# Optimization experiments

Measured on AMD Instinct MI355X. Metric: run time of the kernel, lower is better.

Reference implementation:

```python
import jax, jax.numpy as jnp
import numpy as np

B = 524288  # number of mel frames
MEL = 128   # mel bins (hard-coded in module)
D = 64      # code dim
K = 128     # codebook size


def setup_inputs() -> dict:
    key = jax.random.key(0)
    ks = jax.random.split(key, 7)
    return {
        "mel_frame": jax.random.normal(ks[0], (B, MEL), dtype=jnp.float32),
        "W_in": jax.random.normal(ks[1], (D, MEL), dtype=jnp.float32) * 0.05,
        "b_in": jax.random.normal(ks[2], (D,), dtype=jnp.float32) * 0.05,
        "cb0": jax.random.normal(ks[3], (K, D), dtype=jnp.float32),
        "cb1": jax.random.normal(ks[4], (K, D), dtype=jnp.float32),
        "W_out": jax.random.normal(ks[5], (MEL, D), dtype=jnp.float32) * 0.05,
        "b_out": jax.random.normal(ks[6], (MEL,), dtype=jnp.float32) * 0.05,
    }


def reference(mel_frame, W_in, b_in, cb0, cb1, W_out, b_out):
    # encode: project mel -> d, then greedy residual VQ over 2 codebooks
    z = mel_frame @ W_in.T + b_in                      # (B, D)
    residual = z
    z_q = jnp.zeros_like(z)
    idxs = []
    for cb in (cb0, cb1):
        # squared L2 distance without materializing (B, K, D):
        # ||r - c||^2 = ||r||^2 - 2 r.c + ||c||^2  -> (B, K)
        dist = (
            jnp.sum(residual * residual, axis=-1, keepdims=True)
            - 2.0 * (residual @ cb.T)
            + jnp.sum(cb * cb, axis=-1)
        )
        ind = jnp.argmin(dist, axis=-1)                # (B,)
        code = cb[ind]                                 # gather chosen codes (B, D)
        residual = residual - code
        z_q = z_q + code
        idxs.append(ind)
    # decode: sum of selected codes -> project back to mel
    mel = z_q @ W_out.T + b_out                        # (B, MEL)
    return mel, jnp.stack(idxs, axis=-1)
```

## Files before the change

### kernel.cpp

```cpp
#include <hip/hip_runtime.h>
#include <hip/hip_bf16.h>

#define B_ROWS   524288
#define MEL_BINS 128
#define DIM      64
#define KCODES   128

#define WS_WT  0
#define WS_PL0 (WS_WT + 8192)
#define WS_PS0 (WS_PL0 + 4096)
#define WS_PL1 (WS_PS0 + 4096)
#define WS_PS1 (WS_PL1 + 4096)
#define WS_N0  (WS_PS1 + 4096)
#define WS_N1  (WS_N0 + KCODES)
#define WS_T0  (WS_N1 + KCODES)
#define WS_T1  (WS_T0 + KCODES*MEL_BINS)
#define WS_TOT (WS_T1 + KCODES*MEL_BINS)

__device__ __forceinline__ float np_pairwise64_sq(const float* v) {
#pragma clang fp contract(off)
    float r0 = v[0]*v[0], r1 = v[1]*v[1], r2 = v[2]*v[2], r3 = v[3]*v[3];
    float r4 = v[4]*v[4], r5 = v[5]*v[5], r6 = v[6]*v[6], r7 = v[7]*v[7];
#pragma unroll
    for (int i = 8; i < 64; i += 8) {
        r0 += v[i+0]*v[i+0]; r1 += v[i+1]*v[i+1];
        r2 += v[i+2]*v[i+2]; r3 += v[i+3]*v[i+3];
        r4 += v[i+4]*v[i+4]; r5 += v[i+5]*v[i+5];
        r6 += v[i+6]*v[i+6]; r7 += v[i+7]*v[i+7];
    }
    return ((r0 + r1) + (r2 + r3)) + ((r4 + r5) + (r6 + r7));
}

__global__ __launch_bounds__(256) void rvq_precomp(
    const float* __restrict__ W_in, const float* __restrict__ cb0,
    const float* __restrict__ cb1, const float* __restrict__ W_out,
    float* __restrict__ ws)
{
#pragma clang fp contract(off)
    float* WT  = ws + WS_WT;
    float* PL0 = ws + WS_PL0;
    float* PS0 = ws + WS_PS0;
    float* PL1 = ws + WS_PL1;
    float* PS1 = ws + WS_PS1;
    float* n0  = ws + WS_N0;
    float* n1  = ws + WS_N1;
    float* T0  = ws + WS_T0;
    float* T1  = ws + WS_T1;

    int tid = blockIdx.x * 256 + threadIdx.x;
    if (tid < 16384) {
        int i = tid >> 7, m = tid & 127;
        double a = 0.0;
        for (int d = 0; d < DIM; ++d)
            a = fma((double)cb0[i*DIM + d], (double)W_out[m*DIM + d], a);
        T0[tid] = (float)a;
    } else if (tid < 32768) {
        int t = tid - 16384;
        int i = t >> 7, m = t & 127;
        double a = 0.0;
        for (int d = 0; d < DIM; ++d)
            a = fma((double)cb1[i*DIM + d], (double)W_out[m*DIM + d], a);
        T1[t] = (float)a;
    } else if (tid < 40960) {
        int t = tid - 32768;
        int j = t >> 6, d = t & 63;
        WT[t] = W_in[d*MEL_BINS + j];
    } else if (tid < 41216) {
        int t = tid - 40960;
        const float* cb = (t & 128) ? cb1 : cb0;
        float*       nn = (t & 128) ? n1  : n0;
        int k = t & 127;
        nn[k] = np_pairwise64_sq(cb + k*DIM);
    } else if (tid < 49408) {
        int e = tid - 41216;
        int half = e >> 12;
        int x = e & 4095;
        int c = x >> 9, rem = x & 511;
        int d = rem >> 3, t = rem & 7;
        if (half == 0) PL0[x] = cb0[(16*c + t)*DIM + d];
        else           PS0[x] = cb0[(16*c + 8 + t)*DIM + d];
    } else if (tid < 57600) {
        int e = tid - 49408;
        int half = e >> 12;
        int x = e & 4095;
        int c = x >> 9, rem = x & 511;
        int d = rem >> 3, t = rem & 7;
        if (half == 0) PL1[x] = cb1[(16*c + t)*DIM + d];
        else           PS1[x] = cb1[(16*c + 8 + t)*DIM + d];
    }
}

__global__ __launch_bounds__(256, 3) void rvq_main(
    const float* __restrict__ mel,
    const float* __restrict__ b_in,
    const float* __restrict__ cb0,
    const float* __restrict__ cb1,
    const float* __restrict__ b_out,
    const float* __restrict__ ws,
    float* __restrict__ out_mel,
    float* __restrict__ out_idx)
{
#pragma clang fp contract(off)
    const float* __restrict__ ps0g = ws + WS_PS0;
    const float* __restrict__ ps1g = ws + WS_PS1;
    const float* __restrict__ n0g  = ws + WS_N0;
    const float* __restrict__ n1g  = ws + WS_N1;
    const float* __restrict__ T0   = ws + WS_T0;
    const float* __restrict__ T1   = ws + WS_T1;

    __shared__ float slds[4096];
    float4* sw4 = reinterpret_cast<float4*>(slds);
    const float4* sl4 = reinterpret_cast<const float4*>(slds);

    const int tid = threadIdx.x;
    const int b = blockIdx.x * 256 + tid;
    const float4* melr = reinterpret_cast<const float4*>(mel + (size_t)b * MEL_BINS);

    float z[DIM];
#pragma unroll
    for (int d = 0; d < DIM; ++d) z[d] = 0.f;

    const float4* wt4 = reinterpret_cast<const float4*>(ws + WS_WT);
    for (int h = 0; h < 2; ++h) {
        __syncthreads();
#pragma unroll
        for (int i = 0; i < 4; ++i) sw4[i*256 + tid] = wt4[h*1024 + i*256 + tid];
        __syncthreads();

        for (int jc = 0; jc < 16; ++jc) {
            float4 m4 = melr[h*16 + jc];
#pragma unroll
            for (int seg = 0; seg < 4; ++seg) {
                float mj = (seg == 0) ? m4.x : (seg == 1) ? m4.y : (seg == 2) ? m4.z : m4.w;
                const float4* w4 = sl4 + (jc*4 + seg)*16;
#pragma unroll
                for (int q = 0; q < 16; ++q) {
                    float4 wv = w4[q];
                    z[4*q + 0] = fmaf(wv.x, mj, z[4*q + 0]);
                    z[4*q + 1] = fmaf(wv.y, mj, z[4*q + 1]);
                    z[4*q + 2] = fmaf(wv.z, mj, z[4*q + 2]);
                    z[4*q + 3] = fmaf(wv.w, mj, z[4*q + 3]);
                }
            }
        }
    }
#pragma unroll
    for (int d = 0; d < DIM; ++d) z[d] = z[d] + b_in[d];

    float s0 = z[0]*z[0], s1 = z[1]*z[1], s2 = z[2]*z[2], s3 = z[3]*z[3];
    float s4 = z[4]*z[4], s5 = z[5]*z[5], s6 = z[6]*z[6], s7 = z[7]*z[7];
#pragma unroll
    for (int i = 8; i < 64; i += 8) {
        s0 += z[i+0]*z[i+0]; s1 += z[i+1]*z[i+1];
        s2 += z[i+2]*z[i+2]; s3 += z[i+3]*z[i+3];
        s4 += z[i+4]*z[i+4]; s5 += z[i+5]*z[i+5];
        s6 += z[i+6]*z[i+6]; s7 += z[i+7]*z[i+7];
    }
    float sum_rr = ((s0 + s1) + (s2 + s3)) + ((s4 + s5) + (s6 + s7));

    const float4* pl04 = reinterpret_cast<const float4*>(ws + WS_PL0);
    float best0 = 3.4e38f; int i0 = 0;
    __syncthreads();
#pragma unroll
    for (int i = 0; i < 4; ++i) sw4[i*256 + tid] = pl04[i*256 + tid];
    __syncthreads();

    for (int c = 0; c < 8; ++c) {
        const float4* pan  = sl4 + c*128;
        const float* srow  = ps0g + c*512;
        float acc[16];
#pragma unroll
        for (int t = 0; t < 16; ++t) acc[t] = 0.f;
#pragma unroll
        for (int d = 0; d < DIM; ++d) {
            float4 p0 = pan[d*2 + 0];
            float4 p1 = pan[d*2 + 1];
            const float* sr = srow + d*8;
            float zd = z[d];
            acc[ 0] = fmaf(p0.x, zd, acc[ 0]);
            acc[ 1] = fmaf(p0.y, zd, acc[ 1]);
            acc[ 2] = fmaf(p0.z, zd, acc[ 2]);
            acc[ 3] = fmaf(p0.w, zd, acc[ 3]);
            acc[ 4] = fmaf(p1.x, zd, acc[ 4]);
            acc[ 5] = fmaf(p1.y, zd, acc[ 5]);
            acc[ 6] = fmaf(p1.z, zd, acc[ 6]);
            acc[ 7] = fmaf(p1.w, zd, acc[ 7]);
            acc[ 8] = fmaf(sr[0], zd, acc[ 8]);
            acc[ 9] = fmaf(sr[1], zd, acc[ 9]);
            acc[10] = fmaf(sr[2], zd, acc[10]);
            acc[11] = fmaf(sr[3], zd, acc[11]);
            acc[12] = fmaf(sr[4], zd, acc[12]);
            acc[13] = fmaf(sr[5], zd, acc[13]);
            acc[14] = fmaf(sr[6], zd, acc[14]);
            acc[15] = fmaf(sr[7], zd, acc[15]);
        }
        const int kb = c*16;
        const float* nk = n0g + kb;
#pragma unroll
        for (int t = 0; t < 16; ++t) {
            float dist = (sum_rr - 2.0f*acc[t]) + nk[t];
            if (dist < best0) { best0 = dist; i0 = kb + t; }
        }
    }

    {
        const float* cc = cb0 + (size_t)i0 * DIM;
#pragma unroll
        for (int d = 0; d < DIM; ++d) z[d] = z[d] - cc[d];
    }

    s0 = z[0]*z[0]; s1 = z[1]*z[1]; s2 = z[2]*z[2]; s3 = z[3]*z[3];
    s4 = z[4]*z[4]; s5 = z[5]*z[5]; s6 = z[6]*z[6]; s7 = z[7]*z[7];
#pragma unroll
    for (int i = 8; i < 64; i += 8) {
        s0 += z[i+0]*z[i+0]; s1 += z[i+1]*z[i+1];
        s2 += z[i+2]*z[i+2]; s3 += z[i+3]*z[i+3];
        s4 += z[i+4]*z[i+4]; s5 += z[i+5]*z[i+5];
        s6 += z[i+6]*z[i+6]; s7 += z[i+7]*z[i+7];
    }
    sum_rr = ((s0 + s1) + (s2 + s3)) + ((s4 + s5) + (s6 + s7));

    const float4* pl14 = reinterpret_cast<const float4*>(ws + WS_PL1);
    float best1 = 3.4e38f; int i1 = 0;
    __syncthreads();
#pragma unroll
    for (int i = 0; i < 4; ++i) sw4[i*256 + tid] = pl14[i*256 + tid];
    __syncthreads();

    for (int c = 0; c < 8; ++c) {
        const float4* pan  = sl4 + c*128;
        const float* srow  = ps1g + c*512;
        float acc[16];
#pragma unroll
        for (int t = 0; t < 16; ++t) acc[t] = 0.f;
#pragma unroll
        for (int d = 0; d < DIM; ++d) {
            float4 p0 = pan[d*2 + 0];
            float4 p1 = pan[d*2 + 1];
            const float* sr = srow + d*8;
            float zd = z[d];
            acc[ 0] = fmaf(p0.x, zd, acc[ 0]);
            acc[ 1] = fmaf(p0.y, zd, acc[ 1]);
            acc[ 2] = fmaf(p0.z, zd, acc[ 2]);
            acc[ 3] = fmaf(p0.w, zd, acc[ 3]);
            acc[ 4] = fmaf(p1.x, zd, acc[ 4]);
            acc[ 5] = fmaf(p1.y, zd, acc[ 5]);
            acc[ 6] = fmaf(p1.z, zd, acc[ 6]);
            acc[ 7] = fmaf(p1.w, zd, acc[ 7]);
            acc[ 8] = fmaf(sr[0], zd, acc[ 8]);
            acc[ 9] = fmaf(sr[1], zd, acc[ 9]);
            acc[10] = fmaf(sr[2], zd, acc[10]);
            acc[11] = fmaf(sr[3], zd, acc[11]);
            acc[12] = fmaf(sr[4], zd, acc[12]);
            acc[13] = fmaf(sr[5], zd, acc[13]);
            acc[14] = fmaf(sr[6], zd, acc[14]);
            acc[15] = fmaf(sr[7], zd, acc[15]);
        }
        const int kb = c*16;
        const float* nk = n1g + kb;
#pragma unroll
        for (int t = 0; t < 16; ++t) {
            float dist = (sum_rr - 2.0f*acc[t]) + nk[t];
            if (dist < best1) { best1 = dist; i1 = kb + t; }
        }
    }

    const float4* t0r = reinterpret_cast<const float4*>(T0 + (size_t)i0 * MEL_BINS);
    const float4* t1r = reinterpret_cast<const float4*>(T1 + (size_t)i1 * MEL_BINS);
    float4* outr = reinterpret_cast<float4*>(out_mel + (size_t)b * MEL_BINS);
#pragma unroll 4
    for (int q = 0; q < MEL_BINS / 4; ++q) {
        float4 a = t0r[q], cc = t1r[q];
        float4 o;
        o.x = a.x + cc.x + b_out[4*q + 0];
        o.y = a.y + cc.y + b_out[4*q + 1];
        o.z = a.z + cc.z + b_out[4*q + 2];
        o.w = a.w + cc.w + b_out[4*q + 3];
        outr[q] = o;
    }

    out_idx[2*(size_t)b + 0] = (float)i0;
    out_idx[2*(size_t)b + 1] = (float)i1;
}

extern "C" void kernel_launch(void* const* d_in, const int* in_sizes, int n_in,
                              void* d_out, int out_size, void* d_ws, size_t ws_size,
                              hipStream_t stream)
{
    const float* mel   = (const float*)d_in[0];
    const float* W_in  = (const float*)d_in[1];
    const float* b_in  = (const float*)d_in[2];
    const float* cb0   = (const float*)d_in[3];
    const float* cb1   = (const float*)d_in[4];
    const float* W_out = (const float*)d_in[5];
    const float* b_out = (const float*)d_in[6];

    float* ws      = (float*)d_ws;
    float* out_mel = (float*)d_out;
    float* out_idx = (float*)d_out + (size_t)B_ROWS * MEL_BINS;

    rvq_precomp<<<(WS_TOT + 255) / 256, 256, 0, stream>>>(W_in, cb0, cb1, W_out, ws);
    rvq_main<<<B_ROWS / 256, 256, 0, stream>>>(mel, b_in, cb0, cb1, b_out, ws,
                                               out_mel, out_idx);
}
```

Measured before the change: 489.5 us.

## Split input projection into separate GEMM kernel writing z to workspace

Moves the mel-to-z projection out of the main kernel into a dedicated kernel. It stages 64 mel rows in padded LDS and writes z to workspace in a transposed float4-planar layout. The VQ/decode kernel then reads z coalesced instead of recomputing it, with the original fused kernel kept as a fallback when the workspace is too small. This is meant to cut register pressure and the strided per-thread mel reads, at the cost of an extra 128 MB write and read round trip of z through HBM.

```diff
diff --git a/kernel.cpp b/kernel.cpp
--- a/kernel.cpp
+++ b/kernel.cpp
@@ -16,6 +16,7 @@
 #define WS_T0  (WS_N1 + KCODES)
 #define WS_T1  (WS_T0 + KCODES*MEL_BINS)
 #define WS_TOT (WS_T1 + KCODES*MEL_BINS)
+#define WS_Z   WS_TOT
 
 __device__ __forceinline__ float np_pairwise64_sq(const float* v) {
 #pragma clang fp contract(off)
@@ -90,13 +91,65 @@
     }
 }
 
-__global__ __launch_bounds__(256, 3) void rvq_main(
+__global__ __launch_bounds__(256) void rvq_zgemm(
     const float* __restrict__ mel,
     const float* __restrict__ b_in,
+    const float* __restrict__ ws,
+    float* __restrict__ zws)
+{
+#pragma clang fp contract(off)
+    __shared__ float smel[64 * 129];
+
+    const int tid = threadIdx.x;
+    const int w = tid >> 6, l = tid & 63;
+    const size_t rowbase = (size_t)blockIdx.x * 64;
+
+    const float4* mg = reinterpret_cast<const float4*>(mel + rowbase * MEL_BINS);
+#pragma unroll
+    for (int q = 0; q < 8; ++q) {
+        int idx = tid * 8 + q;
+        int r = idx >> 5, c = idx & 31;
+        float4 v = mg[idx];
+        smel[r*129 + 4*c + 0] = v.x;
+        smel[r*129 + 4*c + 1] = v.y;
+        smel[r*129 + 4*c + 2] = v.z;
+        smel[r*129 + 4*c + 3] = v.w;
+    }
+    __syncthreads();
+
+    const float* WTw = ws + WS_WT + w * 16;
+    float zz[16];
+#pragma unroll
+    for (int t = 0; t < 16; ++t) zz[t] = 0.f;
+
+#pragma unroll 4
+    for (int j = 0; j < 128; ++j) {
+        float m = smel[l*129 + j];
+        const float* wt = WTw + j * 64;
+#pragma unroll
+        for (int t = 0; t < 16; ++t) zz[t] = fmaf(wt[t], m, zz[t]);
+    }
+    const float* bi = b_in + w * 16;
+#pragma unroll
+    for (int t = 0; t < 16; ++t) zz[t] = zz[t] + bi[t];
+
+    float4* zo = reinterpret_cast<float4*>(zws);
+    const size_t r = rowbase + l;
+#pragma unroll
+    for (int qq = 0; qq < 4; ++qq) {
+        float4 v;
+        v.x = zz[4*qq + 0]; v.y = zz[4*qq + 1];
+        v.z = zz[4*qq + 2]; v.w = zz[4*qq + 3];
+        zo[(size_t)(w*4 + qq) * B_ROWS + r] = v;
+    }
+}
+
+__global__ __launch_bounds__(256) void rvq_dots(
     const float* __restrict__ cb0,
     const float* __restrict__ cb1,
     const float* __restrict__ b_out,
     const float* __restrict__ ws,
+    const float* __restrict__ zws,
     float* __restrict__ out_mel,
     float* __restrict__ out_idx)
 {
@@ -113,39 +166,18 @@
     const float4* sl4 = reinterpret_cast<const float4*>(slds);
 
     const int tid = threadIdx.x;
-    const int b = blockIdx.x * 256 + tid;
-    const float4* melr = reinterpret_cast<const float4*>(mel + (size_t)b * MEL_BINS);
+    const size_t b = (size_t)blockIdx.x * 256 + tid;
 
     float z[DIM];
-#pragma unroll
-    for (int d = 0; d < DIM; ++d) z[d] = 0.f;
-
-    const float4* wt4 = reinterpret_cast<const float4*>(ws + WS_WT);
-    for (int h = 0; h < 2; ++h) {
-        __syncthreads();
-#pragma unroll
-        for (int i = 0; i < 4; ++i) sw4[i*256 + tid] = wt4[h*1024 + i*256 + tid];
-        __syncthreads();
-
-        for (int jc = 0; jc < 16; ++jc) {
-            float4 m4 = melr[h*16 + jc];
-#pragma unroll
-            for (int seg = 0; seg < 4; ++seg) {
-                float mj = (seg == 0) ? m4.x : (seg == 1) ? m4.y : (seg == 2) ? m4.z : m4.w;
-                const float4* w4 = sl4 + (jc*4 + seg)*16;
-#pragma unroll
-                for (int q = 0; q < 16; ++q) {
-                    float4 wv = w4[q];
-                    z[4*q + 0] = fmaf(wv.x, mj, z[4*q + 0]);
-                    z[4*q + 1] = fmaf(wv.y, mj, z[4*q + 1]);
-                    z[4*q + 2] = fmaf(wv.z, mj, z[4*q + 2]);
-                    z[4*q + 3] = fmaf(wv.w, mj, z[4*q + 3]);
-                }
-            }
-        }
-    }
-#pragma unroll
-    for (int d = 0; d < DIM; ++d) z[d] = z[d] + b_in[d];
+    {
+        const float4* zi = reinterpret_cast<const float4*>(zws);
+#pragma unroll
+        for (int q = 0; q < 16; ++q) {
+            float4 v = zi[(size_t)q * B_ROWS + b];
+            z[4*q + 0] = v.x; z[4*q + 1] = v.y;
+            z[4*q + 2] = v.z; z[4*q + 3] = v.w;
+        }
+    }
 
     float s0 = z[0]*z[0], s1 = z[1]*z[1], s2 = z[2]*z[2], s3 = z[3]*z[3];
     float s4 = z[4]*z[4], s5 = z[5]*z[5], s6 = z[6]*z[6], s7 = z[7]*z[7];
@@ -160,7 +192,6 @@
 
     const float4* pl04 = reinterpret_cast<const float4*>(ws + WS_PL0);
     float best0 = 3.4e38f; int i0 = 0;
-    __syncthreads();
 #pragma unroll
     for (int i = 0; i < 4; ++i) sw4[i*256 + tid] = pl04[i*256 + tid];
     __syncthreads();
@@ -267,6 +298,198 @@
 
     const float4* t0r = reinterpret_cast<const float4*>(T0 + (size_t)i0 * MEL_BINS);
     const float4* t1r = reinterpret_cast<const float4*>(T1 + (size_t)i1 * MEL_BINS);
+    float4* outr = reinterpret_cast<float4*>(out_mel + b * MEL_BINS);
+#pragma unroll 4
+    for (int q = 0; q < MEL_BINS / 4; ++q) {
+        float4 a = t0r[q], cc = t1r[q];
+        float4 o;
+        o.x = a.x + cc.x + b_out[4*q + 0];
+        o.y = a.y + cc.y + b_out[4*q + 1];
+        o.z = a.z + cc.z + b_out[4*q + 2];
+        o.w = a.w + cc.w + b_out[4*q + 3];
+        outr[q] = o;
+    }
+
+    out_idx[2*b + 0] = (float)i0;
+    out_idx[2*b + 1] = (float)i1;
+}
+
+__global__ __launch_bounds__(256) void rvq_main_fb(
+    const float* __restrict__ mel,
+    const float* __restrict__ b_in,
+    const float* __restrict__ cb0,
+    const float* __restrict__ cb1,
+    const float* __restrict__ b_out,
+    const float* __restrict__ ws,
+    float* __restrict__ out_mel,
+    float* __restrict__ out_idx)
+{
+#pragma clang fp contract(off)
+    const float* __restrict__ ps0g = ws + WS_PS0;
+    const float* __restrict__ ps1g = ws + WS_PS1;
+    const float* __restrict__ n0g  = ws + WS_N0;
+    const float* __restrict__ n1g  = ws + WS_N1;
+    const float* __restrict__ T0   = ws + WS_T0;
+    const float* __restrict__ T1   = ws + WS_T1;
+
+    __shared__ float slds[4096];
+    float4* sw4 = reinterpret_cast<float4*>(slds);
+    const float4* sl4 = reinterpret_cast<const float4*>(slds);
+
+    const int tid = threadIdx.x;
+    const int b = blockIdx.x * 256 + tid;
+    const float4* melr = reinterpret_cast<const float4*>(mel + (size_t)b * MEL_BINS);
+
+    float z[DIM];
+#pragma unroll
+    for (int d = 0; d < DIM; ++d) z[d] = 0.f;
+
+    const float4* wt4 = reinterpret_cast<const float4*>(ws + WS_WT);
+    for (int h = 0; h < 2; ++h) {
+        __syncthreads();
+#pragma unroll
+        for (int i = 0; i < 4; ++i) sw4[i*256 + tid] = wt4[h*1024 + i*256 + tid];
+        __syncthreads();
+        for (int jc = 0; jc < 16; ++jc) {
+            float4 m4 = melr[h*16 + jc];
+#pragma unroll
+            for (int seg = 0; seg < 4; ++seg) {
+                float mj = (seg == 0) ? m4.x : (seg == 1) ? m4.y : (seg == 2) ? m4.z : m4.w;
+                const float4* w4 = sl4 + (jc*4 + seg)*16;
+#pragma unroll
+                for (int q = 0; q < 16; ++q) {
+                    float4 wv = w4[q];
+                    z[4*q + 0] = fmaf(wv.x, mj, z[4*q + 0]);
+                    z[4*q + 1] = fmaf(wv.y, mj, z[4*q + 1]);
+                    z[4*q + 2] = fmaf(wv.z, mj, z[4*q + 2]);
+                    z[4*q + 3] = fmaf(wv.w, mj, z[4*q + 3]);
+                }
+            }
+        }
+    }
+#pragma unroll
+    for (int d = 0; d < DIM; ++d) z[d] = z[d] + b_in[d];
+
+    float s0 = z[0]*z[0], s1 = z[1]*z[1], s2 = z[2]*z[2], s3 = z[3]*z[3];
+    float s4 = z[4]*z[4], s5 = z[5]*z[5], s6 = z[6]*z[6], s7 = z[7]*z[7];
+#pragma unroll
+    for (int i = 8; i < 64; i += 8) {
+        s0 += z[i+0]*z[i+0]; s1 += z[i+1]*z[i+1];
+        s2 += z[i+2]*z[i+2]; s3 += z[i+3]*z[i+3];
+        s4 += z[i+4]*z[i+4]; s5 += z[i+5]*z[i+5];
+        s6 += z[i+6]*z[i+6]; s7 += z[i+7]*z[i+7];
+    }
+    float sum_rr = ((s0 + s1) + (s2 + s3)) + ((s4 + s5) + (s6 + s7));
+
+    const float4* pl04 = reinterpret_cast<const float4*>(ws + WS_PL0);
+    float best0 = 3.4e38f; int i0 = 0;
+    __syncthreads();
+#pragma unroll
+    for (int i = 0; i < 4; ++i) sw4[i*256 + tid] = pl04[i*256 + tid];
+    __syncthreads();
+
+    for (int c = 0; c < 8; ++c) {
+        const float4* pan  = sl4 + c*128;
+        const float* srow  = ps0g + c*512;
+        float acc[16];
+#pragma unroll
+        for (int t = 0; t < 16; ++t) acc[t] = 0.f;
+#pragma unroll
+        for (int d = 0; d < DIM; ++d) {
+            float4 p0 = pan[d*2 + 0];
+            float4 p1 = pan[d*2 + 1];
+            const float* sr = srow + d*8;
+            float zd = z[d];
+            acc[ 0] = fmaf(p0.x, zd, acc[ 0]);
+            acc[ 1] = fmaf(p0.y, zd, acc[ 1]);
+            acc[ 2] = fmaf(p0.z, zd, acc[ 2]);
+            acc[ 3] = fmaf(p0.w, zd, acc[ 3]);
+            acc[ 4] = fmaf(p1.x, zd, acc[ 4]);
+            acc[ 5] = fmaf(p1.y, zd, acc[ 5]);
+            acc[ 6] = fmaf(p1.z, zd, acc[ 6]);
+            acc[ 7] = fmaf(p1.w, zd, acc[ 7]);
+            acc[ 8] = fmaf(sr[0], zd, acc[ 8]);
+            acc[ 9] = fmaf(sr[1], zd, acc[ 9]);
+            acc[10] = fmaf(sr[2], zd, acc[10]);
+            acc[11] = fmaf(sr[3], zd, acc[11]);
+            acc[12] = fmaf(sr[4], zd, acc[12]);
+            acc[13] = fmaf(sr[5], zd, acc[13]);
+            acc[14] = fmaf(sr[6], zd, acc[14]);
+            acc[15] = fmaf(sr[7], zd, acc[15]);
+        }
+        const int kb = c*16;
+        const float* nk = n0g + kb;
+#pragma unroll
+        for (int t = 0; t < 16; ++t) {
+            float dist = (sum_rr - 2.0f*acc[t]) + nk[t];
+            if (dist < best0) { best0 = dist; i0 = kb + t; }
+        }
+    }
+
+    {
+        const float* cc = cb0 + (size_t)i0 * DIM;
+#pragma unroll
+        for (int d = 0; d < DIM; ++d) z[d] = z[d] - cc[d];
+    }
+
+    s0 = z[0]*z[0]; s1 = z[1]*z[1]; s2 = z[2]*z[2]; s3 = z[3]*z[3];
+    s4 = z[4]*z[4]; s5 = z[5]*z[5]; s6 = z[6]*z[6]; s7 = z[7]*z[7];
+#pragma unroll
+    for (int i = 8; i < 64; i += 8) {
+        s0 += z[i+0]*z[i+0]; s1 += z[i+1]*z[i+1];
+        s2 += z[i+2]*z[i+2]; s3 += z[i+3]*z[i+3];
+        s4 += z[i+4]*z[i+4]; s5 += z[i+5]*z[i+5];
+        s6 += z[i+6]*z[i+6]; s7 += z[i+7]*z[i+7];
+    }
+    sum_rr = ((s0 + s1) + (s2 + s3)) + ((s4 + s5) + (s6 + s7));
+
+    const float4* pl14 = reinterpret_cast<const float4*>(ws + WS_PL1);
+    float best1 = 3.4e38f; int i1 = 0;
+    __syncthreads();
+#pragma unroll
+    for (int i = 0; i < 4; ++i) sw4[i*256 + tid] = pl14[i*256 + tid];
+    __syncthreads();
+
+    for (int c = 0; c < 8; ++c) {
+        const float4* pan  = sl4 + c*128;
+        const float* srow  = ps1g + c*512;
+        float acc[16];
+#pragma unroll
+        for (int t = 0; t < 16; ++t) acc[t] = 0.f;
+#pragma unroll
+        for (int d = 0; d < DIM; ++d) {
+            float4 p0 = pan[d*2 + 0];
+            float4 p1 = pan[d*2 + 1];
+            const float* sr = srow + d*8;
+            float zd = z[d];
+            acc[ 0] = fmaf(p0.x, zd, acc[ 0]);
+            acc[ 1] = fmaf(p0.y, zd, acc[ 1]);
+            acc[ 2] = fmaf(p0.z, zd, acc[ 2]);
+            acc[ 3] = fmaf(p0.w, zd, acc[ 3]);
+            acc[ 4] = fmaf(p1.x, zd, acc[ 4]);
+            acc[ 5] = fmaf(p1.y, zd, acc[ 5]);
+            acc[ 6] = fmaf(p1.z, zd, acc[ 6]);
+            acc[ 7] = fmaf(p1.w, zd, acc[ 7]);
+            acc[ 8] = fmaf(sr[0], zd, acc[ 8]);
+            acc[ 9] = fmaf(sr[1], zd, acc[ 9]);
+            acc[10] = fmaf(sr[2], zd, acc[10]);
+            acc[11] = fmaf(sr[3], zd, acc[11]);
+            acc[12] = fmaf(sr[4], zd, acc[12]);
+            acc[13] = fmaf(sr[5], zd, acc[13]);
+            acc[14] = fmaf(sr[6], zd, acc[14]);
+            acc[15] = fmaf(sr[7], zd, acc[15]);
+        }
+        const int kb = c*16;
+        const float* nk = n1g + kb;
+#pragma unroll
+        for (int t = 0; t < 16; ++t) {
+            float dist = (sum_rr - 2.0f*acc[t]) + nk[t];
+            if (dist < best1) { best1 = dist; i1 = kb + t; }
+        }
+    }
+
+    const float4* t0r = reinterpret_cast<const float4*>(T0 + (size_t)i0 * MEL_BINS);
+    const float4* t1r = reinterpret_cast<const float4*>(T1 + (size_t)i1 * MEL_BINS);
     float4* outr = reinterpret_cast<float4*>(out_mel + (size_t)b * MEL_BINS);
 #pragma unroll 4
     for (int q = 0; q < MEL_BINS / 4; ++q) {
@@ -300,6 +523,15 @@
     float* out_idx = (float*)d_out + (size_t)B_ROWS * MEL_BINS;
 
     rvq_precomp<<<(WS_TOT + 255) / 256, 256, 0, stream>>>(W_in, cb0, cb1, W_out, ws);
-    rvq_main<<<B_ROWS / 256, 256, 0, stream>>>(mel, b_in, cb0, cb1, b_out, ws,
-                                               out_mel, out_idx);
+
+    const size_t need = (size_t)WS_TOT * 4 + (size_t)B_ROWS * DIM * 4;
+    if (ws_size >= need) {
+        float* zws = ws + WS_Z;
+        rvq_zgemm<<<B_ROWS / 64, 256, 0, stream>>>(mel, b_in, ws, zws);
+        rvq_dots<<<B_ROWS / 256, 256, 0, stream>>>(cb0, cb1, b_out, ws, zws,
+                                                   out_mel, out_idx);
+    } else {
+        rvq_main_fb<<<B_ROWS / 256, 256, 0, stream>>>(mel, b_in, cb0, cb1, b_out,
+                                                      ws, out_mel, out_idx);
+    }
 }
```

New measurement: 911.9 us. 86.3% more time.
